# Performance work log

Hardware: AMD Instinct MI355X
Metric: run time of the kernel (lower is better)

The kernel has to match this reference:

```python
import jax, jax.numpy as jnp
import numpy as np

B, T, D, H = 512, 2048, 256, 256  # batch, seq_len, input_size, hidden_size


def _uniform(key, shape, fan_in):
    b = 1.0 / np.sqrt(fan_in)
    return jax.random.uniform(key, shape, minval=-b, maxval=b, dtype=jnp.float32)


def setup_inputs() -> dict:
    key = jax.random.key(0)
    ks = jax.random.split(key, 12)
    return {
        "input_tensor": jax.random.normal(ks[0], (B, T, D), dtype=jnp.float32),
        # fc_i: Linear(D, D)
        "Wi": _uniform(ks[1], (D, D), D), "bi": _uniform(ks[2], (D,), D),
        # fc_h: Linear(H, H)
        "Wh": _uniform(ks[3], (H, H), H), "bh": _uniform(ks[4], (H,), H),
        # fc_a: Linear(D, D)
        "Wa": _uniform(ks[5], (D, D), D), "ba": _uniform(ks[6], (D,), D),
        # LSTM(input_size=D, hidden_size=H), gates ordered [i, f, g, o]
        "W_ih": _uniform(ks[7], (4 * H, D), H), "b_ih": _uniform(ks[8], (4 * H,), H),
        "W_hh": _uniform(ks[9], (4 * H, H), H), "b_hh": _uniform(ks[10], (4 * H,), H),
    }


def reference(input_tensor, Wi, bi, Wh, bh, Wa, ba, W_ih, W_hh, b_ih, b_hh):
    x = input_tensor                      # (B, T, D)
    Bb = x.shape[0]
    Hh = Wh.shape[0]
    h0 = jnp.zeros((Bb, Hh), x.dtype)
    c0 = jnp.zeros((Bb, Hh), x.dtype)

    # Per-timestep FC attention; hidden state never updates in the loop,
    # so it vectorizes exactly over T.
    input_o = jnp.einsum('btd,ed->bte', x, Wi) + bi          # (B, T, D)
    hidden_o = h0 @ Wh.T + bh                                # (B, H) == (B, D)
    pre = input_o + hidden_o[:, None, :]                     # (B, T, D)
    attn = jax.nn.sigmoid(jnp.einsum('btd,ed->bte', pre, Wa) + ba)
    attention_output = jnp.sum(attn * x, axis=1)             # (B, D)

    # LSTM over a length-1 sequence (single cell step), PyTorch gate order i,f,g,o
    gates = attention_output @ W_ih.T + b_ih + h0 @ W_hh.T + b_hh
    i, f, g, o = jnp.split(gates, 4, axis=-1)
    i = jax.nn.sigmoid(i); f = jax.nn.sigmoid(f)
    g = jnp.tanh(g); o = jax.nn.sigmoid(o)
    c = f * c0 + i * g
    h = o * jnp.tanh(c)

    lstm_output = h[None]                                    # (1, B, H)
    return (lstm_output, h[None], c[None])
```

## Files before the change

### kernel.cpp

```cpp
#include <hip/hip_runtime.h>
#include <hip/hip_bf16.h>

typedef _Float16 f16x8 __attribute__((ext_vector_type(8)));
typedef float    f32x4 __attribute__((ext_vector_type(4)));

#define B_SZ 512
#define T_SZ 2048
#define D_SZ 256
#define TCHUNK 16
#define NCHUNK (T_SZ / TCHUNK)

__global__ __launch_bounds__(256) void prep_kernel(
    const float* __restrict__ Wa, const float* __restrict__ Wi,
    const float* __restrict__ bi, const float* __restrict__ bh,
    const float* __restrict__ ba,
    _Float16* __restrict__ Weff, float* __restrict__ beff)
{
    int e = blockIdx.x;
    int d = threadIdx.x;
    float a0 = 0.f, a1 = 0.f, a2 = 0.f, a3 = 0.f;
    #pragma unroll 4
    for (int k = 0; k < 256; k += 4) {
        a0 = fmaf(Wa[e*256 + k    ], Wi[(k    )*256 + d], a0);
        a1 = fmaf(Wa[e*256 + k + 1], Wi[(k + 1)*256 + d], a1);
        a2 = fmaf(Wa[e*256 + k + 2], Wi[(k + 2)*256 + d], a2);
        a3 = fmaf(Wa[e*256 + k + 3], Wi[(k + 3)*256 + d], a3);
    }
    Weff[e*256 + d] = (_Float16)((a0 + a1) + (a2 + a3));

    __shared__ float red[4];
    float s = Wa[e*256 + d] * (bi[d] + bh[d]);
    s += __shfl_down(s, 32, 64);
    s += __shfl_down(s, 16, 64);
    s += __shfl_down(s,  8, 64);
    s += __shfl_down(s,  4, 64);
    s += __shfl_down(s,  2, 64);
    s += __shfl_down(s,  1, 64);
    if ((d & 63) == 0) red[d >> 6] = s;
    __syncthreads();
    if (d == 0) beff[e] = ba[e] + ((red[0] + red[1]) + (red[2] + red[3]));
}

__global__ __launch_bounds__(512, 4) void attn_kernel(
    const float* __restrict__ x,
    const _Float16* __restrict__ Weff,
    const float* __restrict__ beff,
    float* __restrict__ ao)
{
    const int b    = blockIdx.x;
    const int tid  = threadIdx.x;
    const int wave = tid >> 6;
    const int lane = tid & 63;
    const int l15  = lane & 15;
    const int lq   = lane >> 4;

    __shared__ _Float16 xs[TCHUNK * 256];
    char* xsb = reinterpret_cast<char*>(xs);

    const int col0 = wave*32 + l15;
    const int col1 = col0 + 16;
    f16x8 bfA[8], bfB[8];
    #pragma unroll
    for (int ks = 0; ks < 8; ++ks) {
        bfA[ks] = *reinterpret_cast<const f16x8*>(&Weff[col0*256 + ks*32 + lq*8]);
        bfB[ks] = *reinterpret_cast<const f16x8*>(&Weff[col1*256 + ks*32 + lq*8]);
    }
    const float bc0 = beff[col0];
    const float bc1 = beff[col1];

    const float* xb = x + (size_t)b * T_SZ * D_SZ;

    const int srow = tid >> 5;
    const int scg  = tid & 31;
    const float* srcp = xb + (size_t)srow * 256 + scg * 8;
    const int swb = (srow*512 + scg*16) ^ ((srow & 7) << 4);

    #define LOADC(R, c)                                                            \
        {                                                                          \
            const float* p = srcp + (size_t)(c) * (TCHUNK * D_SZ);                 \
            R##0 = *reinterpret_cast<const f32x4*>(p);                             \
            R##1 = *reinterpret_cast<const f32x4*>(p + 4);                         \
        }

    #define WRITE(R)                                                               \
        {                                                                          \
            f16x8 h;                                                               \
            h[0] = (_Float16)R##0[0]; h[1] = (_Float16)R##0[1];                    \
            h[2] = (_Float16)R##0[2]; h[3] = (_Float16)R##0[3];                    \
            h[4] = (_Float16)R##1[0]; h[5] = (_Float16)R##1[1];                    \
            h[6] = (_Float16)R##1[2]; h[7] = (_Float16)R##1[3];                    \
            *reinterpret_cast<f16x8*>(xsb + swb) = h;                              \
        }

    #define SYNC()                                                                 \
        {                                                                          \
            asm volatile("s_waitcnt lgkmcnt(0)" ::: "memory");                     \
            __builtin_amdgcn_sched_barrier(0);                                     \
            __builtin_amdgcn_s_barrier();                                          \
        }

    #define COMPUTE()                                                              \
        {                                                                          \
            const int arow  = l15;                                                 \
            const int aswz  = (arow & 7) << 4;                                     \
            const int abase = arow * 512;                                          \
            f32x4 acc0 = {0.f, 0.f, 0.f, 0.f};                                     \
            f32x4 acc1 = {0.f, 0.f, 0.f, 0.f};                                     \
            _Pragma("unroll")                                                      \
            for (int ks = 0; ks < 8; ++ks) {                                       \
                int ab = abase + ((ks*64 + lq*16) ^ aswz);                         \
                f16x8 a = *reinterpret_cast<const f16x8*>(xsb + ab);               \
                acc0 = __builtin_amdgcn_mfma_f32_16x16x32_f16(a, bfA[ks], acc0, 0, 0, 0); \
                acc1 = __builtin_amdgcn_mfma_f32_16x16x32_f16(a, bfB[ks], acc1, 0, 0, 0); \
            }                                                                      \
            _Pragma("unroll")                                                      \
            for (int r = 0; r < 4; ++r) {                                          \
                int row  = lq*4 + r;                                               \
                int rswz = (row & 7) << 4;                                         \
                int rb   = row * 512;                                              \
                {                                                                  \
                    float s = acc0[r] + bc0;                                       \
                    float attn = __builtin_amdgcn_rcpf(1.f + __expf(-s));          \
                    float xv = (float)*reinterpret_cast<const _Float16*>(          \
                        xsb + rb + ((col0*2) ^ rswz));                             \
                    ao0 = fmaf(attn, xv, ao0);                                     \
                }                                                                  \
                {                                                                  \
                    float s = acc1[r] + bc1;                                       \
                    float attn = __builtin_amdgcn_rcpf(1.f + __expf(-s));          \
                    float xv = (float)*reinterpret_cast<const _Float16*>(          \
                        xsb + rb + ((col1*2) ^ rswz));                             \
                    ao1 = fmaf(attn, xv, ao1);                                     \
                }                                                                  \
            }                                                                      \
        }

    float ao0 = 0.f, ao1 = 0.f;
    f32x4 sA0, sA1, sB0, sB1;

    LOADC(sA, 0);
    LOADC(sB, 1);

    for (int c = 0; c < NCHUNK; c += 2) {
        WRITE(sA);
        SYNC();
        if (c + 2 < NCHUNK) LOADC(sA, c + 2);
        COMPUTE();
        SYNC();
        WRITE(sB);
        SYNC();
        if (c + 3 < NCHUNK) LOADC(sB, c + 3);
        COMPUTE();
        SYNC();
    }

    ao0 += __shfl_xor(ao0, 16, 64);
    ao0 += __shfl_xor(ao0, 32, 64);
    ao1 += __shfl_xor(ao1, 16, 64);
    ao1 += __shfl_xor(ao1, 32, 64);
    if (lq == 0) {
        ao[b*256 + col0] = ao0;
        ao[b*256 + col1] = ao1;
    }

    #undef LOADC
    #undef WRITE
    #undef SYNC
    #undef COMPUTE
}

__global__ __launch_bounds__(256) void lstm_kernel(
    const float* __restrict__ ao,
    const float* __restrict__ Wih,
    const float* __restrict__ bih,
    const float* __restrict__ bhh,
    float* __restrict__ out)
{
    int b = blockIdx.x;
    int j = threadIdx.x;
    __shared__ float a[256];
    a[j] = ao[b*256 + j];
    __syncthreads();

    float gi = bih[j]       + bhh[j];
    float gg = bih[512 + j] + bhh[512 + j];
    float go = bih[768 + j] + bhh[768 + j];
    const float* wi = Wih + (size_t)j * 256;
    const float* wg = Wih + (size_t)(512 + j) * 256;
    const float* wo = Wih + (size_t)(768 + j) * 256;
    #pragma unroll 4
    for (int k = 0; k < 256; k += 4) {
        f32x4 w1 = *reinterpret_cast<const f32x4*>(wi + k);
        f32x4 w2 = *reinterpret_cast<const f32x4*>(wg + k);
        f32x4 w3 = *reinterpret_cast<const f32x4*>(wo + k);
        #pragma unroll
        for (int q = 0; q < 4; ++q) {
            float av = a[k + q];
            gi = fmaf(w1[q], av, gi);
            gg = fmaf(w2[q], av, gg);
            go = fmaf(w3[q], av, go);
        }
    }
    float ig = 1.f / (1.f + __expf(-gi));
    float g  = tanhf(gg);
    float og = 1.f / (1.f + __expf(-go));
    float cc = ig * g;
    float hh = og * tanhf(cc);
    out[          b*256 + j] = hh;
    out[131072 +  b*256 + j] = hh;
    out[262144 +  b*256 + j] = cc;
}

extern "C" void kernel_launch(void* const* d_in, const int* in_sizes, int n_in,
                              void* d_out, int out_size, void* d_ws, size_t ws_size,
                              hipStream_t stream) {
    const float* x    = (const float*)d_in[0];
    const float* Wi   = (const float*)d_in[1];
    const float* bi   = (const float*)d_in[2];
    const float* bh   = (const float*)d_in[4];
    const float* Wa   = (const float*)d_in[5];
    const float* ba   = (const float*)d_in[6];
    const float* W_ih = (const float*)d_in[7];
    const float* b_ih = (const float*)d_in[8];
    const float* b_hh = (const float*)d_in[10];

    char* ws = (char*)d_ws;
    _Float16* Weff = (_Float16*)ws;
    float*    beff = (float*)(ws + 128*1024);
    float*    ao   = (float*)(ws + 132*1024);

    prep_kernel<<<256, 256, 0, stream>>>(Wa, Wi, bi, bh, ba, Weff, beff);
    attn_kernel<<<B_SZ, 512, 0, stream>>>(x, Weff, beff, ao);
    lstm_kernel<<<B_SZ, 256, 0, stream>>>(ao, W_ih, b_ih, b_hh, (float*)d_out);
}
```

Before: 264.8 us.

## Double-buffer LDS chunks and transpose MFMA output for vectorized epilogue

```diff
diff --git a/kernel.cpp b/kernel.cpp
--- a/kernel.cpp
+++ b/kernel.cpp
@@ -2,6 +2,7 @@
 #include <hip/hip_bf16.h>
 
 typedef _Float16 f16x8 __attribute__((ext_vector_type(8)));
+typedef _Float16 f16x4 __attribute__((ext_vector_type(4)));
 typedef float    f32x4 __attribute__((ext_vector_type(4)));
 
 #define B_SZ 512
@@ -54,8 +55,9 @@
     const int l15  = lane & 15;
     const int lq   = lane >> 4;
 
-    __shared__ _Float16 xs[TCHUNK * 256];
-    char* xsb = reinterpret_cast<char*>(xs);
+    __shared__ _Float16 xs[2][TCHUNK * 256];
+    char* xsb0 = reinterpret_cast<char*>(&xs[0][0]);
+    char* xsb1 = reinterpret_cast<char*>(&xs[1][0]);
 
     const int col0 = wave*32 + l15;
     const int col1 = col0 + 16;
@@ -65,8 +67,8 @@
         bfA[ks] = *reinterpret_cast<const f16x8*>(&Weff[col0*256 + ks*32 + lq*8]);
         bfB[ks] = *reinterpret_cast<const f16x8*>(&Weff[col1*256 + ks*32 + lq*8]);
     }
-    const float bc0 = beff[col0];
-    const float bc1 = beff[col1];
+    const f32x4 bcA = *reinterpret_cast<const f32x4*>(&beff[wave*32 + lq*4]);
+    const f32x4 bcB = *reinterpret_cast<const f32x4*>(&beff[wave*32 + 16 + lq*4]);
 
     const float* xb = x + (size_t)b * T_SZ * D_SZ;
 
@@ -82,14 +84,14 @@
             R##1 = *reinterpret_cast<const f32x4*>(p + 4);                         \
         }
 
-    #define WRITE(R)                                                               \
+    #define WRITE(BUF, R)                                                          \
         {                                                                          \
             f16x8 h;                                                               \
             h[0] = (_Float16)R##0[0]; h[1] = (_Float16)R##0[1];                    \
             h[2] = (_Float16)R##0[2]; h[3] = (_Float16)R##0[3];                    \
             h[4] = (_Float16)R##1[0]; h[5] = (_Float16)R##1[1];                    \
             h[6] = (_Float16)R##1[2]; h[7] = (_Float16)R##1[3];                    \
-            *reinterpret_cast<f16x8*>(xsb + swb) = h;                              \
+            *reinterpret_cast<f16x8*>((BUF) + swb) = h;                            \
         }
 
     #define SYNC()                                                                 \
@@ -99,68 +101,68 @@
             __builtin_amdgcn_s_barrier();                                          \
         }
 
-    #define COMPUTE()                                                              \
-        {                                                                          \
-            const int arow  = l15;                                                 \
-            const int aswz  = (arow & 7) << 4;                                     \
-            const int abase = arow * 512;                                          \
+    #define COMPUTE(BUF)                                                           \
+        {                                                                          \
+            const int aswz  = (l15 & 7) << 4;                                      \
+            const int abase = l15 * 512;                                           \
             f32x4 acc0 = {0.f, 0.f, 0.f, 0.f};                                     \
             f32x4 acc1 = {0.f, 0.f, 0.f, 0.f};                                     \
             _Pragma("unroll")                                                      \
             for (int ks = 0; ks < 8; ++ks) {                                       \
                 int ab = abase + ((ks*64 + lq*16) ^ aswz);                         \
-                f16x8 a = *reinterpret_cast<const f16x8*>(xsb + ab);               \
-                acc0 = __builtin_amdgcn_mfma_f32_16x16x32_f16(a, bfA[ks], acc0, 0, 0, 0); \
-                acc1 = __builtin_amdgcn_mfma_f32_16x16x32_f16(a, bfB[ks], acc1, 0, 0, 0); \
+                f16x8 a = *reinterpret_cast<const f16x8*>((BUF) + ab);             \
+                acc0 = __builtin_amdgcn_mfma_f32_16x16x32_f16(bfA[ks], a, acc0, 0, 0, 0); \
+                acc1 = __builtin_amdgcn_mfma_f32_16x16x32_f16(bfB[ks], a, acc1, 0, 0, 0); \
             }                                                                      \
+             \
+            int eb0 = abase + (((wave*64      ) + lq*8) ^ aswz);                   \
+            int eb1 = abase + (((wave*64 + 32 ) + lq*8) ^ aswz);                   \
+            f16x4 xq0 = *reinterpret_cast<const f16x4*>((BUF) + eb0);              \
+            f16x4 xq1 = *reinterpret_cast<const f16x4*>((BUF) + eb1);              \
             _Pragma("unroll")                                                      \
             for (int r = 0; r < 4; ++r) {                                          \
-                int row  = lq*4 + r;                                               \
-                int rswz = (row & 7) << 4;                                         \
-                int rb   = row * 512;                                              \
                 {                                                                  \
-                    float s = acc0[r] + bc0;                                       \
+                    float s = acc0[r] + bcA[r];                                    \
                     float attn = __builtin_amdgcn_rcpf(1.f + __expf(-s));          \
-                    float xv = (float)*reinterpret_cast<const _Float16*>(          \
-                        xsb + rb + ((col0*2) ^ rswz));                             \
-                    ao0 = fmaf(attn, xv, ao0);                                     \
+                    ao0[r] = fmaf(attn, (float)xq0[r], ao0[r]);                    \
                 }                                                                  \
                 {                                                                  \
-                    float s = acc1[r] + bc1;                                       \
+                    float s = acc1[r] + bcB[r];                                    \
                     float attn = __builtin_amdgcn_rcpf(1.f + __expf(-s));          \
-                    float xv = (float)*reinterpret_cast<const _Float16*>(          \
-                        xsb + rb + ((col1*2) ^ rswz));                             \
-                    ao1 = fmaf(attn, xv, ao1);                                     \
+                    ao1[r] = fmaf(attn, (float)xq1[r], ao1[r]);                    \
                 }                                                                  \
             }                                                                      \
         }
 
-    float ao0 = 0.f, ao1 = 0.f;
+    f32x4 ao0 = {0.f, 0.f, 0.f, 0.f};
+    f32x4 ao1 = {0.f, 0.f, 0.f, 0.f};
     f32x4 sA0, sA1, sB0, sB1;
 
     LOADC(sA, 0);
     LOADC(sB, 1);
 
     for (int c = 0; c < NCHUNK; c += 2) {
-        WRITE(sA);
+        WRITE(xsb0, sA);
         SYNC();
         if (c + 2 < NCHUNK) LOADC(sA, c + 2);
-        COMPUTE();
-        SYNC();
-        WRITE(sB);
+        COMPUTE(xsb0);
+        WRITE(xsb1, sB);
         SYNC();
         if (c + 3 < NCHUNK) LOADC(sB, c + 3);
-        COMPUTE();
-        SYNC();
-    }
-
-    ao0 += __shfl_xor(ao0, 16, 64);
-    ao0 += __shfl_xor(ao0, 32, 64);
-    ao1 += __shfl_xor(ao1, 16, 64);
-    ao1 += __shfl_xor(ao1, 32, 64);
-    if (lq == 0) {
-        ao[b*256 + col0] = ao0;
-        ao[b*256 + col1] = ao1;
+        COMPUTE(xsb1);
+    }
+
+    #pragma unroll
+    for (int m = 1; m <= 8; m <<= 1) {
+        #pragma unroll
+        for (int r = 0; r < 4; ++r) {
+            ao0[r] += __shfl_xor(ao0[r], m, 64);
+            ao1[r] += __shfl_xor(ao1[r], m, 64);
+        }
+    }
+    if (l15 == 0) {
+        *reinterpret_cast<f32x4*>(&ao[b*256 + wave*32 +      lq*4]) = ao0;
+        *reinterpret_cast<f32x4*>(&ao[b*256 + wave*32 + 16 + lq*4]) = ao1;
     }
 
     #undef LOADC
```

Result: no change. 264.4 us (-0.1%).
